# Optimization experiments

Measured on AMD Instinct MI355X. Metric: run time of the kernel, lower is better.

## Reference

```python
import jax, jax.numpy as jnp
import numpy as np

NX, DX, H, DO = 8192, 8, 1024, 1


def setup_inputs() -> dict:
    key = jax.random.key(0)
    ks = jax.random.split(key, 7)
    s1 = 1.0 / np.sqrt(DX)  # torch Linear default init bound
    s2 = 1.0 / np.sqrt(H)
    x = jax.random.normal(ks[0], (NX, DX), jnp.float32)
    W1 = jax.random.uniform(ks[1], (H, DX), jnp.float32, -s1, s1)
    b1 = jax.random.uniform(ks[2], (H,), jnp.float32, -s1, s1)
    W2 = jax.random.uniform(ks[3], (H, H), jnp.float32, -s2, s2)
    b2 = jax.random.uniform(ks[4], (H,), jnp.float32, -s2, s2)
    W3 = jax.random.uniform(ks[5], (DO, H), jnp.float32, -s2, s2)
    b3 = jax.random.uniform(ks[6], (DO,), jnp.float32, -s2, s2)
    return {"x": x, "W1": W1, "b1": b1, "W2": W2, "b2": b2, "W3": W3, "b3": b3}


def reference(x, W1, b1, W2, b2, W3, b3):
    # Forward: Linear -> Tanh -> Linear -> Tanh -> Linear
    z1 = jnp.tanh(x @ W1.T + b1)          # [nx, h]
    z2 = jnp.tanh(z1 @ W2.T + b2)         # [nx, h]
    y = z2 @ W3.T + b3                    # [nx, out]

    # DerivTanh(h) = 4/(e^-h + e^h)^2 = sech^2(h) = 1 - tanh(h)^2
    d1 = 1.0 - z1 * z1                    # [nx, h]
    d2 = 1.0 - z2 * z2                    # [nx, h]

    # Vectorized analytic Jacobian (original loops over each input dim k):
    # tmp_k = d2 * (W2 @ (d1 * W1[:, k]))  then  dydx_k = W3 @ tmp_k
    J = d1[:, :, None] * W1[None, :, :]                    # [nx, h, dx]
    J = d2[:, :, None] * jnp.einsum('ij,njk->nik', W2, J)  # [nx, h, dx]
    dydx = jnp.einsum('oj,njk->nok', W3, J)                # [nx, out, dx]
    # Match original list-of-dx ordering: dydx[k] has shape [nx, out]
    dydx = jnp.transpose(dydx, (2, 0, 1))                  # [dx, nx, out]
    return y, dydx
```

## Files before the change

kernel.cpp:

```cpp
#include <hip/hip_runtime.h>
#include <stdint.h>

#define NXS 8192
#define HS  1024

typedef __attribute__((ext_vector_type(8))) short short8;
typedef __attribute__((ext_vector_type(4))) float f32x4;

__device__ __forceinline__ float bf2f(uint32_t b) {
    union { uint32_t u; float f; } c; c.u = b << 16; return c.f;
}
__device__ __forceinline__ uint16_t f2bf(float f) {
    union { float f; uint32_t u; } c; c.f = f;
    return (uint16_t)((c.u + 0x7fffu + ((c.u >> 16) & 1u)) >> 16);
}
__device__ __forceinline__ void async_cp16(const void* g, void* l) {
    __builtin_amdgcn_global_load_lds(
        (const __attribute__((address_space(1))) void*)g,
        (__attribute__((address_space(3))) void*)l,
        16, 0, 0);
}

__global__ __launch_bounds__(256) void k01(
    const float* __restrict__ x, const float* __restrict__ W1,
    const float* __restrict__ b1, const float* __restrict__ W2,
    const float* __restrict__ b3, uint16_t* __restrict__ Z1,
    uint16_t* __restrict__ Bp1, uint16_t* __restrict__ Bp2,
    uint16_t* __restrict__ W1T, float* __restrict__ out)
{
    __shared__ float xs[8][8];
    const int b = blockIdx.x, t = threadIdx.x;
    if (b < 1024) {
        const int n0 = b * 8;
        if (t < 64) xs[t >> 3][t & 7] = x[n0 * 8 + t];
        const int j = t * 4;
        float w[4][8];
#pragma unroll
        for (int c = 0; c < 4; ++c) {
            float4 w0 = *(const float4*)(W1 + (j + c) * 8);
            float4 w1 = *(const float4*)(W1 + (j + c) * 8 + 4);
            w[c][0] = w0.x; w[c][1] = w0.y; w[c][2] = w0.z; w[c][3] = w0.w;
            w[c][4] = w1.x; w[c][5] = w1.y; w[c][6] = w1.z; w[c][7] = w1.w;
        }
        float4 bb = *(const float4*)(b1 + j);
        const float bv[4] = {bb.x, bb.y, bb.z, bb.w};
        __syncthreads();
#pragma unroll
        for (int s = 0; s < 8; ++s) {
            ushort4 o;
            uint16_t* op = (uint16_t*)&o;
#pragma unroll
            for (int c = 0; c < 4; ++c) {
                float sum = bv[c];
#pragma unroll
                for (int k = 0; k < 8; ++k) sum += xs[s][k] * w[c][k];
                op[c] = f2bf(tanhf(sum));
            }
            *(ushort4*)(Z1 + (size_t)(n0 + s) * HS + j) = o;
        }
    } else if (b < 1536) {
        const int tid = (b - 1024) * 256 + t;
        const int l = tid & 63, c = (tid >> 6) & 31, g = tid >> 11;
        const int lr = l & 15, lq = l >> 4;
        const float* src = W2 + (size_t)(g * 16 + lr) * HS + c * 32 + lq * 8;
        float4 a0 = *(const float4*)src;
        float4 a1 = *(const float4*)(src + 4);
        uint16_t o[8];
        o[0] = f2bf(a0.x); o[1] = f2bf(a0.y); o[2] = f2bf(a0.z); o[3] = f2bf(a0.w);
        o[4] = f2bf(a1.x); o[5] = f2bf(a1.y); o[6] = f2bf(a1.z); o[7] = f2bf(a1.w);
        *(ushort4*)(Bp1 + (size_t)tid * 8)     = *(ushort4*)&o[0];
        *(ushort4*)(Bp1 + (size_t)tid * 8 + 4) = *(ushort4*)&o[4];
    } else if (b < 2048) {
        const int tid = (b - 1536) * 256 + t;
        const int l = tid & 63, c = (tid >> 6) & 31, g = tid >> 11;
        const int lr = l & 15, lq = l >> 4;
        uint16_t o[8];
#pragma unroll
        for (int j2 = 0; j2 < 8; ++j2)
            o[j2] = f2bf(W2[(size_t)(c * 32 + lq * 8 + j2) * HS + g * 16 + lr]);
        *(ushort4*)(Bp2 + (size_t)tid * 8)     = *(ushort4*)&o[0];
        *(ushort4*)(Bp2 + (size_t)tid * 8 + 4) = *(ushort4*)&o[4];
    } else if (b < 2336) {
        const int idx = (b - 2048) * 256 + t;
        out[idx] = (idx < NXS) ? b3[0] : 0.f;
    } else {
        const int idx = (b - 2336) * 256 + t;
        const int r = idx >> 10, cc = idx & 1023;
        W1T[idx] = (r < 8) ? f2bf(W1[cc * 8 + r]) : (uint16_t)0;
    }
}

template <int MODE>
__global__ __launch_bounds__(256, 2) void gemm_k(
    const uint16_t* __restrict__ A, const uint16_t* __restrict__ Bp,
    const float* __restrict__ bias, const float* __restrict__ W3,
    uint16_t* __restrict__ Out, float* __restrict__ yOut,
    const uint16_t* __restrict__ Z1, const uint16_t* __restrict__ W1T,
    float* __restrict__ dOut)
{
    constexpr int SMEM_U16 = (MODE == 1) ? 17408 : 16384;
    __shared__ __attribute__((aligned(16))) uint16_t smem[SMEM_U16];
    const int t = threadIdx.x;
    const int wave = t >> 6, lane = t & 63;
    const int lq = lane >> 4, lr = lane & 15;
    const int wr = wave >> 1, wc = wave & 1;
    const int rowBase = blockIdx.x * 128;
    const int colBase = blockIdx.y * 128;

    const uint16_t* gA[4];
#pragma unroll
    for (int i = 0; i < 4; ++i) {
        int s = t + i * 256;
        int rA = s >> 3, qA = (s & 7) ^ (rA & 7);
        gA[i] = A + (size_t)(rowBase + rA) * HS + qA * 8;
    }

    const uint16_t* pB[4];
#pragma unroll
    for (int tj = 0; tj < 4; ++tj)
        pB[tj] = Bp + ((size_t)(colBase >> 4) + wc * 4 + tj) * 16384
                    + (size_t)lane * 8;

    f32x4 acc[4][4] = {};

#pragma unroll
    for (int i = 0; i < 4; ++i)
        async_cp16(gA[i], (char*)smem + t * 16 + i * 4096);
    short8 bc[4][2];
#pragma unroll
    for (int tj = 0; tj < 4; ++tj) {
        bc[tj][0] = *(const short8*)(pB[tj]);
        bc[tj][1] = *(const short8*)(pB[tj] + 512);
    }
    __syncthreads();

    int buf = 0;
    for (int c = 0; c < 16; ++c) {
        short8 bn[4][2];
        if (c < 15) {
#pragma unroll
            for (int i = 0; i < 4; ++i)
                async_cp16(gA[i] + (c + 1) * 64,
                           (char*)smem + (buf ^ 1) * 16384 + t * 16 + i * 4096);
#pragma unroll
            for (int tj = 0; tj < 4; ++tj) {
                bn[tj][0] = *(const short8*)(pB[tj] + (c + 1) * 1024);
                bn[tj][1] = *(const short8*)(pB[tj] + (c + 1) * 1024 + 512);
            }
        }
        const uint16_t* pA = smem + buf * 8192;
#pragma unroll
        for (int kk = 0; kk < 2; ++kk) {
            short8 af[4];
#pragma unroll
            for (int ti = 0; ti < 4; ++ti) {
                int ar = wr * 64 + ti * 16 + lr;
                af[ti] = *(const short8*)(pA + ar * 64
                          + ((((kk << 2) + lq) ^ (ar & 7)) << 3));
            }
#pragma unroll
            for (int ti = 0; ti < 4; ++ti)
#pragma unroll
                for (int tj = 0; tj < 4; ++tj)
                    acc[ti][tj] = __builtin_amdgcn_mfma_f32_16x16x32_bf16(
                        af[ti], bc[tj][kk], acc[ti][tj], 0, 0, 0);
        }
        __syncthreads();
        if (c < 15) {
#pragma unroll
            for (int tj = 0; tj < 4; ++tj) {
                bc[tj][0] = bn[tj][0]; bc[tj][1] = bn[tj][1];
            }
        }
        buf ^= 1;
    }

    if (MODE == 0) {
        float cB[4], cW[4]; int cCol[4];
#pragma unroll
        for (int tj = 0; tj < 4; ++tj) {
            cCol[tj] = colBase + wc * 64 + tj * 16 + lr;
            cB[tj] = bias[cCol[tj]];
            cW[tj] = W3[cCol[tj]];
        }
#pragma unroll
        for (int ti = 0; ti < 4; ++ti) {
#pragma unroll
            for (int r = 0; r < 4; ++r) {
                int row = rowBase + wr * 64 + ti * 16 + lq * 4 + r;
                float ys = 0.f;
#pragma unroll
                for (int tj = 0; tj < 4; ++tj) {
                    float z2 = tanhf(acc[ti][tj][r] + cB[tj]);
                    ys += z2 * cW[tj];
                    Out[(size_t)row * HS + cCol[tj]] = f2bf((1.f - z2 * z2) * cW[tj]);
                }
                ys += __shfl_xor(ys, 1); ys += __shfl_xor(ys, 2);
                ys += __shfl_xor(ys, 4); ys += __shfl_xor(ys, 8);
                if (lr == 0) atomicAdd(&yOut[row], ys);
            }
        }
    } else {
#pragma unroll
        for (int ti = 0; ti < 4; ++ti)
#pragma unroll
            for (int r = 0; r < 4; ++r) {
                int rowl = wr * 64 + ti * 16 + lq * 4 + r;
                const size_t zrow = (size_t)(rowBase + rowl) * HS + colBase;
#pragma unroll
                for (int tj = 0; tj < 4; ++tj) {
                    int coll = wc * 64 + tj * 16 + lr;
                    float z1 = bf2f(Z1[zrow + coll]);
                    smem[rowl * 136 + coll] =
                        f2bf(acc[ti][tj][r] * (1.f - z1 * z1));
                }
            }
        __syncthreads();
        f32x4 dd[2] = {};
#pragma unroll
        for (int h = 0; h < 2; ++h)
#pragma unroll
            for (int kb = 0; kb < 4; ++kb) {
                short8 aF = *(const short8*)(smem + (wave * 32 + h * 16 + lr) * 136
                                             + kb * 32 + lq * 8);
                short8 bF = *(const short8*)(W1T + (size_t)lr * HS + colBase
                                             + kb * 32 + lq * 8);
                dd[h] = __builtin_amdgcn_mfma_f32_16x16x32_bf16(aF, bF, dd[h], 0, 0, 0);
            }
        if (lr < 8) {
#pragma unroll
            for (int h = 0; h < 2; ++h) {
                int row = rowBase + wave * 32 + h * 16 + lq * 4;
#pragma unroll
                for (int rg = 0; rg < 4; ++rg)
                    atomicAdd(&dOut[(size_t)lr * NXS + row + rg], dd[h][rg]);
            }
        }
    }
}

extern "C" void kernel_launch(void* const* d_in, const int* in_sizes, int n_in,
                              void* d_out, int out_size, void* d_ws, size_t ws_size,
                              hipStream_t stream) {
    (void)in_sizes; (void)n_in; (void)out_size; (void)ws_size;
    const float* x  = (const float*)d_in[0];
    const float* W1 = (const float*)d_in[1];
    const float* b1 = (const float*)d_in[2];
    const float* W2 = (const float*)d_in[3];
    const float* b2 = (const float*)d_in[4];
    const float* W3 = (const float*)d_in[5];
    const float* b3 = (const float*)d_in[6];
    float* out = (float*)d_out;

    char* ws = (char*)d_ws;
    uint16_t* Z1  = (uint16_t*)(ws);
    uint16_t* V   = (uint16_t*)(ws + (size_t)16 * 1024 * 1024);
    uint16_t* Bp1 = (uint16_t*)(ws + (size_t)32 * 1024 * 1024);
    uint16_t* Bp2 = (uint16_t*)(ws + (size_t)34 * 1024 * 1024);
    uint16_t* W1T = (uint16_t*)(ws + (size_t)36 * 1024 * 1024);

    k01<<<2400, 256, 0, stream>>>(x, W1, b1, W2, b3, Z1, Bp1, Bp2, W1T, out);
    gemm_k<0><<<dim3(NXS / 128, HS / 128), 256, 0, stream>>>(
        Z1, Bp1, b2, W3, V, out, nullptr, nullptr, nullptr);
    gemm_k<1><<<dim3(NXS / 128, HS / 128), 256, 0, stream>>>(
        V, Bp2, nullptr, nullptr, nullptr, nullptr, Z1, W1T, out + NXS);
}
```

Measured before the change: 138.5 us.

## Unroll GEMM main loop by two with ping-pong B registers and partial vmcnt waits

The K-loop of the bf16 MFMA GEMM is unrolled by two, with separate register sets for B fragments, which removes the per-iteration register copies. Each full __syncthreads, which drains all outstanding memory ops, becomes `s_waitcnt vmcnt(8)` plus a barrier. That waits only for the async A-tile LDS copies, so the next stage's B global loads can stay in flight across the barrier. It relies on the issue order (4 LDS copies before 8 B loads) for correctness, so reordering those loads would break the wait count.

```diff
diff --git a/kernel.cpp b/kernel.cpp
--- a/kernel.cpp
+++ b/kernel.cpp
@@ -19,6 +19,10 @@
         (const __attribute__((address_space(1))) void*)g,
         (__attribute__((address_space(3))) void*)l,
         16, 0, 0);
+}
+__device__ __forceinline__ void wait8_barrier() {
+    asm volatile("s_waitcnt vmcnt(8)" ::: "memory");
+    __builtin_amdgcn_s_barrier();
 }
 
 __global__ __launch_bounds__(256) void k01(
@@ -122,58 +126,66 @@
                     + (size_t)lane * 8;
 
     f32x4 acc[4][4] = {};
-
-#pragma unroll
-    for (int i = 0; i < 4; ++i)
-        async_cp16(gA[i], (char*)smem + t * 16 + i * 4096);
-    short8 bc[4][2];
-#pragma unroll
-    for (int tj = 0; tj < 4; ++tj) {
-        bc[tj][0] = *(const short8*)(pB[tj]);
-        bc[tj][1] = *(const short8*)(pB[tj] + 512);
-    }
-    __syncthreads();
-
-    int buf = 0;
-    for (int c = 0; c < 16; ++c) {
-        short8 bn[4][2];
-        if (c < 15) {
-#pragma unroll
-            for (int i = 0; i < 4; ++i)
-                async_cp16(gA[i] + (c + 1) * 64,
-                           (char*)smem + (buf ^ 1) * 16384 + t * 16 + i * 4096);
-#pragma unroll
-            for (int tj = 0; tj < 4; ++tj) {
-                bn[tj][0] = *(const short8*)(pB[tj] + (c + 1) * 1024);
-                bn[tj][1] = *(const short8*)(pB[tj] + (c + 1) * 1024 + 512);
-            }
-        }
-        const uint16_t* pA = smem + buf * 8192;
-#pragma unroll
-        for (int kk = 0; kk < 2; ++kk) {
-            short8 af[4];
-#pragma unroll
-            for (int ti = 0; ti < 4; ++ti) {
-                int ar = wr * 64 + ti * 16 + lr;
-                af[ti] = *(const short8*)(pA + ar * 64
-                          + ((((kk << 2) + lq) ^ (ar & 7)) << 3));
-            }
-#pragma unroll
-            for (int ti = 0; ti < 4; ++ti)
-#pragma unroll
-                for (int tj = 0; tj < 4; ++tj)
-                    acc[ti][tj] = __builtin_amdgcn_mfma_f32_16x16x32_bf16(
-                        af[ti], bc[tj][kk], acc[ti][tj], 0, 0, 0);
-        }
-        __syncthreads();
-        if (c < 15) {
-#pragma unroll
-            for (int tj = 0; tj < 4; ++tj) {
-                bc[tj][0] = bn[tj][0]; bc[tj][1] = bn[tj][1];
-            }
-        }
-        buf ^= 1;
-    }
+    short8 bX[4][2], bY[4][2];
+
+#define STAGE_TO(bufByte, step)                                              \
+    {                                                                        \
+        _Pragma("unroll")                                                    \
+        for (int k_ = 0; k_ < 4; ++k_)                                       \
+            async_cp16(gA[k_] + (step) * 64,                                 \
+                       (char*)smem + (bufByte) + t * 16 + k_ * 4096);        \
+        asm volatile("" ::: "memory");                                       \
+    }
+#define LOADB(dst, step)                                                     \
+    {                                                                        \
+        _Pragma("unroll")                                                    \
+        for (int tj_ = 0; tj_ < 4; ++tj_) {                                  \
+            dst[tj_][0] = *(const short8*)(pB[tj_] + (step) * 1024);         \
+            dst[tj_][1] = *(const short8*)(pB[tj_] + (step) * 1024 + 512);   \
+        }                                                                    \
+    }
+#define COMPUTE(pAbase, breg)                                                \
+    {                                                                        \
+        const uint16_t* pA_ = (pAbase);                                      \
+        _Pragma("unroll")                                                    \
+        for (int kk_ = 0; kk_ < 2; ++kk_) {                                  \
+            short8 af_[4];                                                   \
+            _Pragma("unroll")                                                \
+            for (int ti_ = 0; ti_ < 4; ++ti_) {                              \
+                int ar_ = wr * 64 + ti_ * 16 + lr;                           \
+                af_[ti_] = *(const short8*)(pA_ + ar_ * 64                   \
+                            + ((((kk_ << 2) + lq) ^ (ar_ & 7)) << 3));       \
+            }                                                                \
+            _Pragma("unroll")                                                \
+            for (int ti_ = 0; ti_ < 4; ++ti_)                                \
+                _Pragma("unroll")                                            \
+                for (int tj_ = 0; tj_ < 4; ++tj_)                            \
+                    acc[ti_][tj_] = __builtin_amdgcn_mfma_f32_16x16x32_bf16( \
+                        af_[ti_], breg[tj_][kk_], acc[ti_][tj_], 0, 0, 0);   \
+        }                                                                    \
+    }
+
+    STAGE_TO(0, 0)
+    LOADB(bX, 0)
+    wait8_barrier();
+
+#pragma unroll 1
+    for (int i = 0; i < 8; ++i) {
+        const int c = 2 * i;
+        STAGE_TO(16384, c + 1)
+        LOADB(bY, c + 1)
+        COMPUTE(smem, bX)
+        wait8_barrier();
+        if (i < 7) {
+            STAGE_TO(0, c + 2)
+            LOADB(bX, c + 2)
+        }
+        COMPUTE(smem + 8192, bY)
+        wait8_barrier();
+    }
+#undef STAGE_TO
+#undef LOADB
+#undef COMPUTE
 
     if (MODE == 0) {
         float cB[4], cW[4]; int cCol[4];
```

New measurement: 141.1 us. No clear change (+1.9%).
